# Kernel tuning notes

Hardware: AMD Instinct MI355X
Metric: run time of the kernel (lower is better)

## Reference

```python
import jax, jax.numpy as jnp
import numpy as np

B, N, E, D, H, O = 4, 10000, 160000, 128, 4, 64
NEG_SLOPE = 0.2  # PyG GATConv default


def setup_inputs() -> dict:
    key = jax.random.key(0)
    ks = jax.random.split(key, 9)
    x = jax.random.normal(ks[0], (B, N, D), jnp.float32)
    edge_index = jax.random.randint(ks[1], (2, E), 0, N, dtype=jnp.int64)
    edge_attr = jax.random.uniform(ks[2], (E,), jnp.float32)
    W_src = jax.random.normal(ks[3], (D, H, O), jnp.float32) * (1.0 / np.sqrt(D))
    att_src = jax.random.normal(ks[4], (H, O), jnp.float32) * 0.1
    att_dst = jax.random.normal(ks[5], (H, O), jnp.float32) * 0.1
    W_edge = jax.random.normal(ks[6], (H, O), jnp.float32) * 0.1  # lin_edge weight for edge_dim=1
    att_edge = jax.random.normal(ks[7], (H, O), jnp.float32) * 0.1
    bias = jnp.zeros((O,), jnp.float32)
    return {"x": x, "edge_index": edge_index, "edge_attr": edge_attr,
            "W_src": W_src, "att_src": att_src, "att_dst": att_dst,
            "W_edge": W_edge, "att_edge": att_edge, "bias": bias}


def reference(x, edge_index, edge_attr, W_src, att_src, att_dst, W_edge, att_edge, bias):
    src, dst = edge_index[0], edge_index[1]
    # shared linear projection (PyG non-bipartite GATConv): [B,N,H,O]
    h = jnp.einsum('bnd,dho->bnho', x, W_src)
    a_src = jnp.einsum('bnho,ho->bnh', h, att_src)  # [B,N,H]
    a_dst = jnp.einsum('bnho,ho->bnh', h, att_dst)  # [B,N,H]
    # edge feature projection (edge_dim=1): [E,H]
    a_edge = edge_attr[:, None] * jnp.einsum('ho,ho->h', W_edge, att_edge)[None, :]
    # attention logits per edge: [B,E,H]
    alpha = a_src[:, src] + a_dst[:, dst] + a_edge[None]
    alpha = jax.nn.leaky_relu(alpha, NEG_SLOPE)
    # segment softmax over destination nodes; segment ops need axis 0 = E
    alpha_t = jnp.transpose(alpha, (1, 0, 2))  # [E,B,H]
    m = jax.ops.segment_max(alpha_t, dst, num_segments=N)  # [N,B,H]
    m = jnp.where(jnp.isfinite(m), m, 0.0)
    p = jnp.exp(alpha_t - m[dst])
    s = jax.ops.segment_sum(p, dst, num_segments=N)
    w = p / jnp.maximum(s[dst], jnp.asarray(1e-16, p.dtype))  # [E,B,H]
    # weighted messages from source nodes, scatter-add into destinations
    msg = w[..., None] * jnp.transpose(h[:, src], (1, 0, 2, 3))  # [E,B,H,O]
    out = jax.ops.segment_sum(msg, dst, num_segments=N)  # [N,B,H,O]
    out = out.mean(axis=2) + bias  # concat=False -> mean over heads, [N,B,O]
    return jnp.transpose(out, (1, 0, 2))  # [B,N,O]
```

## Files before the change

### kernel.cpp

```cpp
#include <hip/hip_runtime.h>
#include <hip/hip_fp16.h>
#include <math.h>

constexpr int B_  = 4;
constexpr int N_  = 10000;
constexpr int E_  = 160000;
constexpr int D_  = 128;
constexpr int H_  = 4;
constexpr int O_  = 64;
constexpr float NEG_SLOPE = 0.2f;
constexpr int CAP = 64;

using half8 = __attribute__((ext_vector_type(8))) _Float16;
using f32x4 = __attribute__((ext_vector_type(4))) float;

static __device__ __forceinline__ unsigned short f2h(float f) {
    return __half_as_ushort(__float2half(f));
}
static __device__ __forceinline__ float h2f(unsigned short u) {
    return __half2float(__ushort_as_half(u));
}

__global__ __launch_bounds__(256) void k_prep(
    const float* __restrict__ Wsrc, const float* __restrict__ att_src,
    const float* __restrict__ att_dst,
    const float* __restrict__ W_edge, const float* __restrict__ att_edge,
    unsigned short* __restrict__ W1t, unsigned short* __restrict__ Vt,
    int* __restrict__ deg, float* __restrict__ c)
{
    const int d = blockIdx.x;
    const int t = threadIdx.x;
    const int h = t >> 6;

    for (int i = d * 256 + t; i < N_; i += 128 * 256) deg[i] = 0;

    const float wv = Wsrc[(size_t)d * 256 + t];
    const int cc = ((t & 63) << 2) | h;
    W1t[(size_t)cc * 128 + d] = f2h(wv);

    float vs = wv * att_src[t];
    float vd = wv * att_dst[t];
#pragma unroll
    for (int off = 32; off > 0; off >>= 1) {
        vs += __shfl_down(vs, off, 64);
        vd += __shfl_down(vd, off, 64);
    }
    if ((t & 63) == 0) {
        Vt[h * 128 + d]       = f2h(vs);
        Vt[(4 + h) * 128 + d] = f2h(vd);
    }
    if (d == 1) {
#pragma unroll
        for (int k = 0; k < 4; ++k) Vt[1024 + k * 256 + t] = 0;
    }

    if (d == 0) {
        float v = W_edge[t] * att_edge[t];
#pragma unroll
        for (int off = 32; off > 0; off >>= 1) v += __shfl_down(v, off, 64);
        if ((t & 63) == 0) c[h] = v;
    }
}

__global__ __launch_bounds__(256) void k_gemm(
    const float* __restrict__ x, const int* __restrict__ ei,
    const float* __restrict__ eattr,
    const unsigned short* __restrict__ W1t, const unsigned short* __restrict__ Vt,
    unsigned short* __restrict__ hbw, float* __restrict__ asrc, float* __restrict__ adst,
    int* __restrict__ deg, int2* __restrict__ srcea)
{
    constexpr int ROWS = 32;
    constexpr int APAD = 136;
    __shared__ uint4 SHq[1024];
    unsigned short* A1 = (unsigned short*)SHq;
    unsigned short* Cb = (unsigned short*)SHq;

    const int t = threadIdx.x;
    const int w = t >> 6;
    const int lane = t & 63;
    const int i = lane & 15;
    const int q = lane >> 4;
    const size_t rowbase = (size_t)blockIdx.x * ROWS;

    half8 breg[4][4];
#pragma unroll
    for (int ks = 0; ks < 4; ++ks)
#pragma unroll
        for (int ctl = 0; ctl < 4; ++ctl) {
            const size_t boff = (size_t)((w * 4 + ctl) * 16 + i) * 128 + ks * 32 + q * 8;
            breg[ks][ctl] = *(const half8*)&W1t[boff];
        }
    half8 vreg[4];
    if (w < 2) {
#pragma unroll
        for (int ks = 0; ks < 4; ++ks)
            vreg[ks] = *(const half8*)&Vt[i * 128 + ks * 32 + q * 8];
    }

    {
        const float4* xg = (const float4*)(x + rowbase * D_);
#pragma unroll
        for (int it = 0; it < 4; ++it) {
            const int idx = it * 256 + t;
            const int row = idx >> 5;
            const int c4  = idx & 31;
            float4 xv = xg[idx];
            ushort4 h1;
            h1.x = f2h(xv.x); h1.y = f2h(xv.y);
            h1.z = f2h(xv.z); h1.w = f2h(xv.w);
            *(ushort4*)&A1[row * APAD + c4 * 4] = h1;
        }
    }
    __syncthreads();

    f32x4 acc[2][4];
#pragma unroll
    for (int tl = 0; tl < 2; ++tl)
#pragma unroll
        for (int ctl = 0; ctl < 4; ++ctl) acc[tl][ctl] = (f32x4){0.f, 0.f, 0.f, 0.f};
    f32x4 accV = (f32x4){0.f, 0.f, 0.f, 0.f};

#pragma unroll
    for (int ks = 0; ks < 4; ++ks) {
        const int a0off = i * APAD + ks * 32 + q * 8;
        const int a1off = (16 + i) * APAD + ks * 32 + q * 8;
        half8 at0 = *(const half8*)&A1[a0off];
        half8 at1 = *(const half8*)&A1[a1off];
#pragma unroll
        for (int ctl = 0; ctl < 4; ++ctl) {
            acc[0][ctl] = __builtin_amdgcn_mfma_f32_16x16x32_f16(at0, breg[ks][ctl], acc[0][ctl], 0, 0, 0);
            acc[1][ctl] = __builtin_amdgcn_mfma_f32_16x16x32_f16(at1, breg[ks][ctl], acc[1][ctl], 0, 0, 0);
        }
        if (w < 2) {
            const half8 atV = (w == 0) ? at0 : at1;
            accV = __builtin_amdgcn_mfma_f32_16x16x32_f16(atV, vreg[ks], accV, 0, 0, 0);
        }
    }

    if (w < 2 && i < 8) {
#pragma unroll
        for (int r = 0; r < 4; ++r) {
            const int row = w * 16 + q * 4 + r;
            const size_t rg = rowbase + row;
            if (i < 4) asrc[rg * 4 + i]       = accV[r];
            else       adst[rg * 4 + (i - 4)] = accV[r];
        }
    }

    __syncthreads();
#pragma unroll
    for (int tl = 0; tl < 2; ++tl) {
#pragma unroll
        for (int ctl = 0; ctl < 4; ++ctl) {
            const int col = (w * 4 + ctl) * 16 + i;
            const int chnk = col >> 3;
            const int within = col & 7;
#pragma unroll
            for (int r = 0; r < 4; ++r) {
                const int row = tl * 16 + q * 4 + r;
                const int s = chnk ^ row;
                Cb[row * 256 + s * 8 + within] = f2h(acc[tl][ctl][r]);
            }
        }
    }
    __syncthreads();
    {
        const int chnk = t & 31;
#pragma unroll
        for (int k = 0; k < 4; ++k) {
            const int row = k * 8 + (t >> 5);
            const int s = chnk ^ row;
            const uint4 v = *(const uint4*)&Cb[row * 256 + s * 8];
            *(uint4*)&hbw[(rowbase + row) * 256 + chnk * 8] = v;
        }
    }

    if (t < 128) {
        const int ee = blockIdx.x * 128 + t;
        const int dstn = ei[E_ + ee];
        const int r = atomicAdd(&deg[dstn], 1);
        srcea[dstn * CAP + r] = make_int2(ei[ee], __float_as_int(eattr[ee]));
    }
}

__global__ __launch_bounds__(256) void k_agg(
    const int* __restrict__ deg, const int2* __restrict__ srcea,
    const float* __restrict__ asrc, const float* __restrict__ adst,
    const float* __restrict__ cvec, const unsigned short* __restrict__ hbu,
    const float* __restrict__ bias, float* __restrict__ out)
{
    __shared__ float pS[4][64][4];
    __shared__ int   baseS[4][64];

    const int b    = blockIdx.x & 3;
    const int g    = blockIdx.x >> 2;
    const int wave = threadIdx.x >> 6;
    const int lane = threadIdx.x & 63;
    const int dst  = g * 4 + wave;

    const int dg   = deg[dst];
    const int ebase = dst * CAP;

    const float4 ad = *(const float4*)&adst[((size_t)b * N_ + dst) * 4];
    const float4 cc = *(const float4*)cvec;

    float a0[4] = {0.f, 0.f, 0.f, 0.f};
    float a1[4] = {0.f, 0.f, 0.f, 0.f};
    float a2[4] = {0.f, 0.f, 0.f, 0.f};
    float a3[4] = {0.f, 0.f, 0.f, 0.f};
    float q0 = 0.f, q1 = 0.f, q2 = 0.f, q3 = 0.f;

    for (int c0 = 0; c0 < dg; c0 += 64) {
        const int jl = c0 + lane;
        const bool valid = jl < dg;
        const int2 rec = srcea[ebase + (valid ? jl : 0)];
        const int   srcl = rec.x;
        const float ea   = __int_as_float(rec.y);
        const float4 as = *(const float4*)&asrc[((size_t)b * N_ + srcl) * 4];
        float4 al;
        al.x = as.x + ad.x + ea * cc.x;
        al.y = as.y + ad.y + ea * cc.y;
        al.z = as.z + ad.z + ea * cc.z;
        al.w = as.w + ad.w + ea * cc.w;
        al.x = al.x > 0.f ? al.x : NEG_SLOPE * al.x;
        al.y = al.y > 0.f ? al.y : NEG_SLOPE * al.y;
        al.z = al.z > 0.f ? al.z : NEG_SLOPE * al.z;
        al.w = al.w > 0.f ? al.w : NEG_SLOPE * al.w;
        const float px = valid ? __expf(al.x) : 0.f;
        const float py = valid ? __expf(al.y) : 0.f;
        const float pz = valid ? __expf(al.z) : 0.f;
        const float pw = valid ? __expf(al.w) : 0.f;
        q0 += px; q1 += py; q2 += pz; q3 += pw;

        *(float4*)&pS[wave][lane][0] = make_float4(px, py, pz, pw);
        baseS[wave][lane] = (b * N_ + srcl) << 8;
        __builtin_amdgcn_wave_barrier();

        const int cnt = min(64, dg - c0);
        const int lo4 = lane * 4;
        int j = 0;
        for (; j + 4 <= cnt; j += 4) {
            const float4 p0 = *(const float4*)&pS[wave][j + 0][0];
            const float4 p1 = *(const float4*)&pS[wave][j + 1][0];
            const float4 p2 = *(const float4*)&pS[wave][j + 2][0];
            const float4 p3 = *(const float4*)&pS[wave][j + 3][0];
            const int r0 = baseS[wave][j + 0];
            const int r1 = baseS[wave][j + 1];
            const int r2 = baseS[wave][j + 2];
            const int r3 = baseS[wave][j + 3];
            const ushort4 h0 = *(const ushort4*)&hbu[(size_t)r0 + lo4];
            const ushort4 h1 = *(const ushort4*)&hbu[(size_t)r1 + lo4];
            const ushort4 h2 = *(const ushort4*)&hbu[(size_t)r2 + lo4];
            const ushort4 h3 = *(const ushort4*)&hbu[(size_t)r3 + lo4];
            a0[0] = fmaf(p0.x, h2f(h0.x), a0[0]);
            a0[1] = fmaf(p0.y, h2f(h0.y), a0[1]);
            a0[2] = fmaf(p0.z, h2f(h0.z), a0[2]);
            a0[3] = fmaf(p0.w, h2f(h0.w), a0[3]);
            a1[0] = fmaf(p1.x, h2f(h1.x), a1[0]);
            a1[1] = fmaf(p1.y, h2f(h1.y), a1[1]);
            a1[2] = fmaf(p1.z, h2f(h1.z), a1[2]);
            a1[3] = fmaf(p1.w, h2f(h1.w), a1[3]);
            a2[0] = fmaf(p2.x, h2f(h2.x), a2[0]);
            a2[1] = fmaf(p2.y, h2f(h2.y), a2[1]);
            a2[2] = fmaf(p2.z, h2f(h2.z), a2[2]);
            a2[3] = fmaf(p2.w, h2f(h2.w), a2[3]);
            a3[0] = fmaf(p3.x, h2f(h3.x), a3[0]);
            a3[1] = fmaf(p3.y, h2f(h3.y), a3[1]);
            a3[2] = fmaf(p3.z, h2f(h3.z), a3[2]);
            a3[3] = fmaf(p3.w, h2f(h3.w), a3[3]);
        }
        for (; j < cnt; ++j) {
            const float4 p0 = *(const float4*)&pS[wave][j][0];
            const int    r0 = baseS[wave][j];
            const ushort4 h0 = *(const ushort4*)&hbu[(size_t)r0 + lo4];
            a0[0] = fmaf(p0.x, h2f(h0.x), a0[0]);
            a0[1] = fmaf(p0.y, h2f(h0.y), a0[1]);
            a0[2] = fmaf(p0.z, h2f(h0.z), a0[2]);
            a0[3] = fmaf(p0.w, h2f(h0.w), a0[3]);
        }
        __builtin_amdgcn_wave_barrier();
    }

#pragma unroll
    for (int off = 32; off > 0; off >>= 1) {
        q0 += __shfl_xor(q0, off, 64);
        q1 += __shfl_xor(q1, off, 64);
        q2 += __shfl_xor(q2, off, 64);
        q3 += __shfl_xor(q3, off, 64);
    }

    const float r = (a0[0] + a1[0] + a2[0] + a3[0]) / fmaxf(q0, 1e-16f)
                  + (a0[1] + a1[1] + a2[1] + a3[1]) / fmaxf(q1, 1e-16f)
                  + (a0[2] + a1[2] + a2[2] + a3[2]) / fmaxf(q2, 1e-16f)
                  + (a0[3] + a1[3] + a2[3] + a3[3]) / fmaxf(q3, 1e-16f);
    out[((size_t)b * N_ + dst) * O_ + lane] = 0.25f * r + bias[lane];
}

extern "C" void kernel_launch(void* const* d_in, const int* in_sizes, int n_in,
                              void* d_out, int out_size, void* d_ws, size_t ws_size,
                              hipStream_t stream)
{
    (void)in_sizes; (void)n_in; (void)out_size; (void)ws_size;
    const float* x        = (const float*)d_in[0];
    const int*   ei       = (const int*)d_in[1];
    const float* eattr    = (const float*)d_in[2];
    const float* Wsrc     = (const float*)d_in[3];
    const float* att_src  = (const float*)d_in[4];
    const float* att_dst  = (const float*)d_in[5];
    const float* W_edge   = (const float*)d_in[6];
    const float* att_edge = (const float*)d_in[7];
    const float* bias     = (const float*)d_in[8];
    float* out = (float*)d_out;

    char* w = (char*)d_ws;
    auto take = [&](size_t bytes) { char* p = w; w += (bytes + 15) & ~size_t(15); return p; };
    unsigned short* hb   = (unsigned short*)take((size_t)B_ * N_ * O_ * H_ * 2);
    float* asrc    = (float*)take((size_t)B_ * N_ * H_ * 4);
    float* adst    = (float*)take((size_t)B_ * N_ * H_ * 4);
    float* c       = (float*)take(4 * 4);
    unsigned short* W1t = (unsigned short*)take((size_t)256 * 128 * 2);
    unsigned short* Vt  = (unsigned short*)take((size_t)16 * 128 * 2);
    int* deg       = (int*)take((size_t)N_ * 4);
    int2* srcea    = (int2*)take((size_t)N_ * CAP * 8);

    hipLaunchKernelGGL(k_prep, dim3(128), dim3(256), 0, stream,
                       Wsrc, att_src, att_dst, W_edge, att_edge,
                       W1t, Vt, deg, c);
    hipLaunchKernelGGL(k_gemm, dim3((B_ * N_) / 32), dim3(256), 0, stream,
                       x, ei, eattr, W1t, Vt, hb, asrc, adst, deg, srcea);
    hipLaunchKernelGGL(k_agg, dim3(N_ / 4 * B_), dim3(256), 0, stream,
                       deg, srcea, asrc, adst, c, hb, bias, out);
}
```

Baseline: 155.6 us.

## Widen aggregation gathers to 16-byte loads and issue edge bucketing earlier

```diff
diff --git a/kernel.cpp b/kernel.cpp
--- a/kernel.cpp
+++ b/kernel.cpp
@@ -11,8 +11,9 @@
 constexpr float NEG_SLOPE = 0.2f;
 constexpr int CAP = 64;
 
-using half8 = __attribute__((ext_vector_type(8))) _Float16;
-using f32x4 = __attribute__((ext_vector_type(4))) float;
+using half8   = __attribute__((ext_vector_type(8))) _Float16;
+using f32x4   = __attribute__((ext_vector_type(4))) float;
+using ushort8v = __attribute__((ext_vector_type(8))) unsigned short;
 
 static __device__ __forceinline__ unsigned short f2h(float f) {
     return __half_as_ushort(__float2half(f));
@@ -82,6 +83,14 @@
     const int q = lane >> 4;
     const size_t rowbase = (size_t)blockIdx.x * ROWS;
 
+    int e_src = 0, e_dst = 0; float e_ea = 0.f;
+    if (t < 128) {
+        const int ee = blockIdx.x * 128 + t;
+        e_dst = ei[E_ + ee];
+        e_src = ei[ee];
+        e_ea  = eattr[ee];
+    }
+
     half8 breg[4][4];
 #pragma unroll
     for (int ks = 0; ks < 4; ++ks)
@@ -113,6 +122,11 @@
     }
     __syncthreads();
 
+    if (t < 128) {
+        const int r = atomicAdd(&deg[e_dst], 1);
+        srcea[e_dst * CAP + r] = make_int2(e_src, __float_as_int(e_ea));
+    }
+
     f32x4 acc[2][4];
 #pragma unroll
     for (int tl = 0; tl < 2; ++tl)
@@ -173,13 +187,6 @@
             const uint4 v = *(const uint4*)&Cb[row * 256 + s * 8];
             *(uint4*)&hbw[(rowbase + row) * 256 + chnk * 8] = v;
         }
-    }
-
-    if (t < 128) {
-        const int ee = blockIdx.x * 128 + t;
-        const int dstn = ei[E_ + ee];
-        const int r = atomicAdd(&deg[dstn], 1);
-        srcea[dstn * CAP + r] = make_int2(ei[ee], __float_as_int(eattr[ee]));
     }
 }
 
@@ -198,16 +205,22 @@
     const int lane = threadIdx.x & 63;
     const int dst  = g * 4 + wave;
 
-    const int dg   = deg[dst];
+    const int dg    = deg[dst];
     const int ebase = dst * CAP;
 
     const float4 ad = *(const float4*)&adst[((size_t)b * N_ + dst) * 4];
     const float4 cc = *(const float4*)cvec;
 
-    float a0[4] = {0.f, 0.f, 0.f, 0.f};
-    float a1[4] = {0.f, 0.f, 0.f, 0.f};
-    float a2[4] = {0.f, 0.f, 0.f, 0.f};
-    float a3[4] = {0.f, 0.f, 0.f, 0.f};
+    const int half = lane >> 5;
+    const int ol   = (lane & 31) * 8;
+
+    float acc[4][2][4];
+#pragma unroll
+    for (int u = 0; u < 4; ++u)
+#pragma unroll
+        for (int oo = 0; oo < 2; ++oo)
+#pragma unroll
+            for (int h = 0; h < 4; ++h) acc[u][oo][h] = 0.f;
     float q0 = 0.f, q1 = 0.f, q2 = 0.f, q3 = 0.f;
 
     for (int c0 = 0; c0 < dg; c0 += 64) {
@@ -237,49 +250,38 @@
         __builtin_amdgcn_wave_barrier();
 
         const int cnt = min(64, dg - c0);
-        const int lo4 = lane * 4;
-        int j = 0;
-        for (; j + 4 <= cnt; j += 4) {
-            const float4 p0 = *(const float4*)&pS[wave][j + 0][0];
-            const float4 p1 = *(const float4*)&pS[wave][j + 1][0];
-            const float4 p2 = *(const float4*)&pS[wave][j + 2][0];
-            const float4 p3 = *(const float4*)&pS[wave][j + 3][0];
-            const int r0 = baseS[wave][j + 0];
-            const int r1 = baseS[wave][j + 1];
-            const int r2 = baseS[wave][j + 2];
-            const int r3 = baseS[wave][j + 3];
-            const ushort4 h0 = *(const ushort4*)&hbu[(size_t)r0 + lo4];
-            const ushort4 h1 = *(const ushort4*)&hbu[(size_t)r1 + lo4];
-            const ushort4 h2 = *(const ushort4*)&hbu[(size_t)r2 + lo4];
-            const ushort4 h3 = *(const ushort4*)&hbu[(size_t)r3 + lo4];
-            a0[0] = fmaf(p0.x, h2f(h0.x), a0[0]);
-            a0[1] = fmaf(p0.y, h2f(h0.y), a0[1]);
-            a0[2] = fmaf(p0.z, h2f(h0.z), a0[2]);
-            a0[3] = fmaf(p0.w, h2f(h0.w), a0[3]);
-            a1[0] = fmaf(p1.x, h2f(h1.x), a1[0]);
-            a1[1] = fmaf(p1.y, h2f(h1.y), a1[1]);
-            a1[2] = fmaf(p1.z, h2f(h1.z), a1[2]);
-            a1[3] = fmaf(p1.w, h2f(h1.w), a1[3]);
-            a2[0] = fmaf(p2.x, h2f(h2.x), a2[0]);
-            a2[1] = fmaf(p2.y, h2f(h2.y), a2[1]);
-            a2[2] = fmaf(p2.z, h2f(h2.z), a2[2]);
-            a2[3] = fmaf(p2.w, h2f(h2.w), a2[3]);
-            a3[0] = fmaf(p3.x, h2f(h3.x), a3[0]);
-            a3[1] = fmaf(p3.y, h2f(h3.y), a3[1]);
-            a3[2] = fmaf(p3.z, h2f(h3.z), a3[2]);
-            a3[3] = fmaf(p3.w, h2f(h3.w), a3[3]);
-        }
-        for (; j < cnt; ++j) {
-            const float4 p0 = *(const float4*)&pS[wave][j][0];
-            const int    r0 = baseS[wave][j];
-            const ushort4 h0 = *(const ushort4*)&hbu[(size_t)r0 + lo4];
-            a0[0] = fmaf(p0.x, h2f(h0.x), a0[0]);
-            a0[1] = fmaf(p0.y, h2f(h0.y), a0[1]);
-            a0[2] = fmaf(p0.z, h2f(h0.z), a0[2]);
-            a0[3] = fmaf(p0.w, h2f(h0.w), a0[3]);
+        for (int j = 0; j < cnt; j += 8) {
+#pragma unroll
+            for (int u = 0; u < 4; ++u) {
+                const int idx = j + 2 * u + half;
+                const float4 p = *(const float4*)&pS[wave][idx][0];
+                const int    r = baseS[wave][idx];
+                const ushort8v hh = *(const ushort8v*)&hbu[(size_t)r + ol];
+                acc[u][0][0] = fmaf(p.x, h2f(hh[0]), acc[u][0][0]);
+                acc[u][0][1] = fmaf(p.y, h2f(hh[1]), acc[u][0][1]);
+                acc[u][0][2] = fmaf(p.z, h2f(hh[2]), acc[u][0][2]);
+                acc[u][0][3] = fmaf(p.w, h2f(hh[3]), acc[u][0][3]);
+                acc[u][1][0] = fmaf(p.x, h2f(hh[4]), acc[u][1][0]);
+                acc[u][1][1] = fmaf(p.y, h2f(hh[5]), acc[u][1][1]);
+                acc[u][1][2] = fmaf(p.z, h2f(hh[6]), acc[u][1][2]);
+                acc[u][1][3] = fmaf(p.w, h2f(hh[7]), acc[u][1][3]);
+            }
         }
         __builtin_amdgcn_wave_barrier();
     }
+
+    float tt[2][4];
+#pragma unroll
+    for (int oo = 0; oo < 2; ++oo)
+#pragma unroll
+        for (int h = 0; h < 4; ++h)
+            tt[oo][h] = (acc[0][oo][h] + acc[1][oo][h]) + (acc[2][oo][h] + acc[3][oo][h]);
+
+#pragma unroll
+    for (int oo = 0; oo < 2; ++oo)
+#pragma unroll
+        for (int h = 0; h < 4; ++h)
+            tt[oo][h] += __shfl_xor(tt[oo][h], 32, 64);
 
 #pragma unroll
     for (int off = 32; off > 0; off >>= 1) {
@@ -289,11 +291,17 @@
         q3 += __shfl_xor(q3, off, 64);
     }
 
-    const float r = (a0[0] + a1[0] + a2[0] + a3[0]) / fmaxf(q0, 1e-16f)
-                  + (a0[1] + a1[1] + a2[1] + a3[1]) / fmaxf(q1, 1e-16f)
-                  + (a0[2] + a1[2] + a2[2] + a3[2]) / fmaxf(q2, 1e-16f)
-                  + (a0[3] + a1[3] + a2[3] + a3[3]) / fmaxf(q3, 1e-16f);
-    out[((size_t)b * N_ + dst) * O_ + lane] = 0.25f * r + bias[lane];
+    if (lane < 32) {
+        const float i0 = 1.f / fmaxf(q0, 1e-16f);
+        const float i1 = 1.f / fmaxf(q1, 1e-16f);
+        const float i2 = 1.f / fmaxf(q2, 1e-16f);
+        const float i3 = 1.f / fmaxf(q3, 1e-16f);
+        const float2 bs = *(const float2*)&bias[lane * 2];
+        float2 res;
+        res.x = 0.25f * (tt[0][0] * i0 + tt[0][1] * i1 + tt[0][2] * i2 + tt[0][3] * i3) + bs.x;
+        res.y = 0.25f * (tt[1][0] * i0 + tt[1][1] * i1 + tt[1][2] * i2 + tt[1][3] * i3) + bs.y;
+        *(float2*)&out[((size_t)b * N_ + dst) * O_ + lane * 2] = res;
+    }
 }
 
 extern "C" void kernel_launch(void* const* d_in, const int* in_sizes, int n_in,
```

Measured after the change: 161.0 us. 3.5% more time.
